# Optimization experiments

Measured on AMD Instinct MI355X. Metric: run time of the kernel, lower is better.

The kernel has to match this reference:

```python
import jax, jax.numpy as jnp
import numpy as np

HIDDEN = 512

def setup_inputs() -> dict:
    key = jax.random.key(0)
    ks = jax.random.split(key, 8)
    S, Bsz, I, H, D = 512, 64, 512, HIDDEN, 2
    return {
        "X": jax.random.normal(ks[0], (S, Bsz, I), jnp.float32),
        "W": jax.random.normal(ks[1], (D, 4 * H, I), jnp.float32) * 0.05,
        "R": jax.random.normal(ks[2], (D, 4 * H, H), jnp.float32) * 0.05,
        "B": jax.random.normal(ks[3], (D, 8 * H), jnp.float32) * 0.05,
        "sequence_lens": jax.random.randint(ks[4], (Bsz,), 0, S, jnp.int32),
        "initial_h": jax.random.normal(ks[5], (D, Bsz, H), jnp.float32) * 0.1,
        "initial_c": jax.random.normal(ks[6], (D, Bsz, H), jnp.float32) * 0.1,
        "P": jax.random.normal(ks[7], (D, 3 * H), jnp.float32) * 0.05,
    }

def _run_dir(Xg, R_d, Rb_d, h0, c0, P_d, seq_lens, ts, H):
    # Gate layout along 4H axis: i, o, f, c (ONNX order used by the source).
    P_i, P_f, P_o = P_d[:H], P_d[H:2 * H], P_d[2 * H:3 * H]

    def step(carry, inp):
        h, c = carry
        xg, t = inp                              # xg: [B,4H] precomputed X@W^T + Wb
        g = xg + h @ R_d.T + Rb_d                # [B,4H]
        i_t = jax.nn.sigmoid(g[:, :H] + P_i * c)
        f_t = jax.nn.sigmoid(g[:, 2 * H:3 * H] + P_f * c)
        c_til = jnp.tanh(g[:, 3 * H:4 * H])
        c_new = f_t * c + i_t * c_til
        o_t = jax.nn.sigmoid(g[:, H:2 * H] + P_o * c_new)
        h_new = o_t * jnp.tanh(c_new)
        mask = (t < seq_lens).astype(h_new.dtype)[:, None]
        h_new = h_new * mask + h0 * (1 - mask)
        c_new = c_new * mask + c0 * (1 - mask)
        return (h_new, c_new), h_new

    (h_f, c_f), hs = jax.lax.scan(step, (h0, c0), (Xg[ts], jnp.asarray(ts)))
    return hs, h_f, c_f

def reference(X, W, R, B, sequence_lens, initial_h, initial_c, P):
    S, Bsz, I = X.shape
    D = W.shape[0]
    H = W.shape[1] // 4
    Wb = B[:, :4 * H]
    Rb = B[:, 4 * H:8 * H]
    # Batch the input projection over all timesteps once: [D,S,B,4H]
    Xg_all = jnp.einsum('sbi,dgi->dsbg', X, W) + Wb[:, None, None, :]
    Ys, Yhs, Ycs = [], [], []
    for d in range(D):
        ts = np.arange(S) if d == 0 else np.arange(S)[::-1].copy()
        hs, h_f, c_f = _run_dir(Xg_all[d], R[d], Rb[d], initial_h[d],
                                initial_c[d], P[d], sequence_lens, ts, H)
        if d == 1:
            hs = hs[::-1]                         # scan emitted reversed time order
        Ys.append(hs)
        Yhs.append(h_f)
        Ycs.append(c_f)
    Y = jnp.stack(Ys, axis=1)                     # [S, D, B, H]
    Y_h = jnp.stack(Yhs, axis=0)                  # [D, B, H]
    Y_c = jnp.stack(Ycs, axis=0)                  # [D, B, H]
    return Y, Y_h, Y_c
```

## Files before the change

kernel.cpp:

```cpp
#include <hip/hip_runtime.h>
#include <stdint.h>
#include <stddef.h>

#define S_LEN 512
#define BATCH 64
#define ISZ   512
#define HID   512
#define NDIR  2

typedef short bf16x8 __attribute__((ext_vector_type(8)));
typedef unsigned short u16x8 __attribute__((ext_vector_type(8)));
typedef float f32x4 __attribute__((ext_vector_type(4)));

#define XB_ELEMS  ((size_t)S_LEN * 4 * 8192)
#define HH_ELEMS  ((size_t)NDIR * 513 * 4 * 8192)
#define CNT_BYTES ((size_t)NDIR * 4 * 513 * 4)
#define XB_BYTES  (XB_ELEMS * 2)
#define HH_BYTES  (HH_ELEMS * 2)

__device__ __forceinline__ unsigned short f2bf(float f) {
    unsigned int u = __float_as_uint(f);
    u += 0x7fffu + ((u >> 16) & 1u);
    return (unsigned short)(u >> 16);
}

__global__ void k_convX(const float* __restrict__ X, unsigned short* __restrict__ Xb) {
    int gu = blockIdx.x * 256 + threadIdx.x;
    int t   = gu >> 12;
    int rem = gu & 4095;
    int b   = rem >> 6;
    int u   = rem & 63;
    const float* src = X + ((size_t)(t * 64 + b)) * 512 + u * 8;
    float4 a = *(const float4*)(src);
    float4 c = *(const float4*)(src + 4);
    u16x8 o;
    o[0]=f2bf(a.x); o[1]=f2bf(a.y); o[2]=f2bf(a.z); o[3]=f2bf(a.w);
    o[4]=f2bf(c.x); o[5]=f2bf(c.y); o[6]=f2bf(c.z); o[7]=f2bf(c.w);
    int i = b >> 4, br = b & 15;
    size_t off = ((size_t)(t * 4 + i)) * 8192 + (size_t)br * 512 + (size_t)((u ^ (b & 7)) << 3);
    *(u16x8*)(Xb + off) = o;
}

__global__ void k_initH(const float* __restrict__ h0, unsigned short* __restrict__ hh) {
    int gu = blockIdx.x * 256 + threadIdx.x;
    int d   = gu >> 12;
    int rem = gu & 4095;
    int b   = rem >> 6;
    int u   = rem & 63;
    const float* src = h0 + ((size_t)(d * 64 + b)) * 512 + u * 8;
    float4 a = *(const float4*)(src);
    float4 c = *(const float4*)(src + 4);
    u16x8 o;
    o[0]=f2bf(a.x); o[1]=f2bf(a.y); o[2]=f2bf(a.z); o[3]=f2bf(a.w);
    o[4]=f2bf(c.x); o[5]=f2bf(c.y); o[6]=f2bf(c.z); o[7]=f2bf(c.w);
    int i = b >> 4, br = b & 15;
    size_t blk = ((size_t)d * 513 + 0) * 4 + i;
    size_t off = blk * 8192 + (size_t)br * 512 + (size_t)((u ^ (b & 7)) << 3);
    *(u16x8*)(hh + off) = o;
}

__launch_bounds__(256, 1)
__global__ void k_lstm(const float* __restrict__ W, const float* __restrict__ R,
                       const float* __restrict__ Bb, const int* __restrict__ slen,
                       const float* __restrict__ h0g, const float* __restrict__ c0g,
                       const float* __restrict__ P,
                       const unsigned short* __restrict__ Xb,
                       unsigned short* __restrict__ hh,
                       int* __restrict__ cnt,
                       float* __restrict__ Y) {
    __shared__ __align__(16) float gbuf[4 * 256];
    __shared__ __align__(4) unsigned short hexch[256];

    const int tid = threadIdx.x;
    const int bx  = blockIdx.x;
    const int d   = bx >> 7;
    const int i   = (bx >> 5) & 3;
    const int j   = bx & 31;
    const int w   = tid >> 6;
    const int l   = tid & 63;
    const int lr  = l & 15;
    const int lq  = l >> 4;

    bf16x8 Wf[16], Rf[16];
    {
        const int row = w * 512 + j * 16 + lr;
        const float* wp = W + ((size_t)(d * 2048 + row)) * 512;
        const float* rp = R + ((size_t)(d * 2048 + row)) * 512;
#pragma unroll
        for (int kc = 0; kc < 16; ++kc) {
            int k0 = kc * 32 + lq * 8;
            float4 a = *(const float4*)(wp + k0);
            float4 b4 = *(const float4*)(wp + k0 + 4);
            bf16x8 f;
            f[0]=(short)f2bf(a.x);  f[1]=(short)f2bf(a.y);  f[2]=(short)f2bf(a.z);  f[3]=(short)f2bf(a.w);
            f[4]=(short)f2bf(b4.x); f[5]=(short)f2bf(b4.y); f[6]=(short)f2bf(b4.z); f[7]=(short)f2bf(b4.w);
            Wf[kc] = f;
            a  = *(const float4*)(rp + k0);
            b4 = *(const float4*)(rp + k0 + 4);
            bf16x8 g;
            g[0]=(short)f2bf(a.x);  g[1]=(short)f2bf(a.y);  g[2]=(short)f2bf(a.z);  g[3]=(short)f2bf(a.w);
            g[4]=(short)f2bf(b4.x); g[5]=(short)f2bf(b4.y); g[6]=(short)f2bf(b4.z); g[7]=(short)f2bf(b4.w);
            Rf[kc] = g;
        }
    }

    const int eb = tid >> 4;
    const int ec = tid & 15;
    const int bg = i * 16 + eb;
    const int kh = j * 16 + ec;
    const float bias_i = Bb[d * 4096 + 0 * 512 + kh] + Bb[d * 4096 + 2048 + 0 * 512 + kh];
    const float bias_o = Bb[d * 4096 + 1 * 512 + kh] + Bb[d * 4096 + 2048 + 1 * 512 + kh];
    const float bias_f = Bb[d * 4096 + 2 * 512 + kh] + Bb[d * 4096 + 2048 + 2 * 512 + kh];
    const float bias_c = Bb[d * 4096 + 3 * 512 + kh] + Bb[d * 4096 + 2048 + 3 * 512 + kh];
    const float Pi = P[d * 1536 + kh];
    const float Pf = P[d * 1536 + 512 + kh];
    const float Po = P[d * 1536 + 1024 + kh];
    const int   sl  = slen[bg];
    const float h0v = h0g[((size_t)d * 64 + bg) * 512 + kh];
    const float c0v = c0g[((size_t)d * 64 + bg) * 512 + kh];
    float c_state = c0v;

    int* mycnt = cnt + (d * 4 + i) * 513;
    const int rbase = lr * 512;
    const int swz   = lr & 7;

    const int peb = tid >> 3;
    const int pm  = tid & 7;
    const size_t puo = (size_t)peb * 256
                     + (size_t)((((2 * j + (pm >> 2)) ^ (peb & 7)) << 2) + (pm & 3));

    for (int ts = 0; ts < 512; ++ts) {
        const int t = (d == 0) ? ts : (511 - ts);

        f32x4 acc = {0.f, 0.f, 0.f, 0.f};
        {
            const unsigned short* xsrc = Xb + ((size_t)(t * 4 + i)) * 8192;
#pragma unroll
            for (int kc = 0; kc < 16; ++kc) {
                int u = (kc * 4 + lq) ^ swz;
                bf16x8 a = *(const bf16x8*)(xsrc + rbase + u * 8);
                acc = __builtin_amdgcn_mfma_f32_16x16x32_bf16(a, Wf[kc], acc, 0, 0, 0);
            }
        }

        if (ts > 0) {
            if (tid == 0) {
                int iters = 0;
                while (__hip_atomic_load(&mycnt[ts], __ATOMIC_RELAXED,
                                         __HIP_MEMORY_SCOPE_AGENT) < 32) {
                    __builtin_amdgcn_s_sleep(1);
                    if (++iters > 4000000) break;
                }
            }
            __syncthreads();
        }

        {
            const unsigned int* hsrc =
                (const unsigned int*)(hh + (((size_t)d * 513 + ts) * 4 + i) * 8192);
            unsigned int hv[64];
#pragma unroll
            for (int kc = 0; kc < 16; ++kc) {
                int u = (kc * 4 + lq) ^ swz;
                const unsigned int* p = hsrc + (lr * 256 + u * 4);
                hv[kc * 4 + 0] = __hip_atomic_load(p + 0, __ATOMIC_RELAXED, __HIP_MEMORY_SCOPE_AGENT);
                hv[kc * 4 + 1] = __hip_atomic_load(p + 1, __ATOMIC_RELAXED, __HIP_MEMORY_SCOPE_AGENT);
                hv[kc * 4 + 2] = __hip_atomic_load(p + 2, __ATOMIC_RELAXED, __HIP_MEMORY_SCOPE_AGENT);
                hv[kc * 4 + 3] = __hip_atomic_load(p + 3, __ATOMIC_RELAXED, __HIP_MEMORY_SCOPE_AGENT);
            }
#pragma unroll
            for (int kc = 0; kc < 16; ++kc) {
                union { unsigned int u[4]; bf16x8 v; } cvt;
                cvt.u[0] = hv[kc * 4 + 0];
                cvt.u[1] = hv[kc * 4 + 1];
                cvt.u[2] = hv[kc * 4 + 2];
                cvt.u[3] = hv[kc * 4 + 3];
                acc = __builtin_amdgcn_mfma_f32_16x16x32_bf16(cvt.v, Rf[kc], acc, 0, 0, 0);
            }
        }

#pragma unroll
        for (int r = 0; r < 4; ++r) {
            int b = lq * 4 + r;
            gbuf[w * 256 + b * 16 + lr] = acc[r];
        }
        __syncthreads();

        float hn, cn;
        {
            float gi = gbuf[0 * 256 + tid] + bias_i;
            float go = gbuf[1 * 256 + tid] + bias_o;
            float gf = gbuf[2 * 256 + tid] + bias_f;
            float gc = gbuf[3 * 256 + tid] + bias_c;
            float c  = c_state;
            float it = 1.f / (1.f + __expf(-(gi + Pi * c)));
            float ft = 1.f / (1.f + __expf(-(gf + Pf * c)));
            float ct = 1.f - 2.f / (__expf(2.f * gc) + 1.f);
            cn = ft * c + it * ct;
            float ot = 1.f / (1.f + __expf(-(go + Po * cn)));
            hn = ot * (1.f - 2.f / (__expf(2.f * cn) + 1.f));
            if (t >= sl) { hn = h0v; cn = c0v; }
            c_state = cn;

            Y[(((size_t)t * 2 + d) * 64 + bg) * 512 + kh] = hn;
            if (ts == 511) {
                Y[(size_t)33554432 + ((size_t)d * 64 + bg) * 512 + kh] = hn;
                Y[(size_t)33619968 + ((size_t)d * 64 + bg) * 512 + kh] = cn;
            }
            hexch[tid] = f2bf(hn);
        }
        __syncthreads();

        if (tid < 128) {
            unsigned int v = ((const unsigned int*)hexch)[tid];
            unsigned int* hdst =
                (unsigned int*)(hh + (((size_t)d * 513 + (ts + 1)) * 4 + i) * 8192);
            __hip_atomic_store(hdst + puo, v, __ATOMIC_RELAXED, __HIP_MEMORY_SCOPE_AGENT);
        }
        asm volatile("s_waitcnt vmcnt(0)" ::: "memory");
        __syncthreads();
        if (tid == 0) {
            __hip_atomic_fetch_add(&mycnt[ts + 1], 1, __ATOMIC_RELAXED,
                                   __HIP_MEMORY_SCOPE_AGENT);
        }
    }
}

extern "C" void kernel_launch(void* const* d_in, const int* in_sizes, int n_in,
                              void* d_out, int out_size, void* d_ws, size_t ws_size,
                              hipStream_t stream) {
    const float* X  = (const float*)d_in[0];
    const float* W  = (const float*)d_in[1];
    const float* R  = (const float*)d_in[2];
    const float* Bb = (const float*)d_in[3];
    const int*   sl = (const int*)d_in[4];
    const float* h0 = (const float*)d_in[5];
    const float* c0 = (const float*)d_in[6];
    const float* P  = (const float*)d_in[7];
    float* Y = (float*)d_out;

    unsigned short* Xb  = (unsigned short*)d_ws;
    unsigned short* hh  = (unsigned short*)((char*)d_ws + XB_BYTES);
    int*            cnt = (int*)((char*)d_ws + XB_BYTES + HH_BYTES);

    hipMemsetAsync(cnt, 0, CNT_BYTES, stream);

    k_convX<<<8192, 256, 0, stream>>>(X, Xb);
    k_initH<<<32, 256, 0, stream>>>(h0, hh);
    k_lstm<<<256, 256, 0, stream>>>(W, R, Bb, sl, h0, c0, P, Xb, hh, cnt, Y);
}
```

Baseline: 4.082 ms.

## Remap LSTM blocks by XCD so each group syncs through its local L2

At kernel start each block reads its hardware XCD id, all blocks meet at a global barrier, and roles are reassigned so that each 32-block group exchanging hidden state sits on the same XCD. When that grouping succeeds, the per-step hidden-state exchange and counter polling use plain loads, stores and workgroup-scope atomics that stay in the XCD's L2, instead of agent-scope atomics that go through device-coherent memory. The per-step counter becomes one monotonically increasing counter per group, and the LDS staging of h is replaced by a lane shuffle that packs bf16 pairs. This adds a startup rendezvous that depends on all 256 blocks being resident at once, and the fast path's correctness relies on the assumption that same-XCD blocks share a coherent L2.

```diff
diff --git a/kernel.cpp b/kernel.cpp
--- a/kernel.cpp
+++ b/kernel.cpp
@@ -14,7 +14,7 @@
 
 #define XB_ELEMS  ((size_t)S_LEN * 4 * 8192)
 #define HH_ELEMS  ((size_t)NDIR * 513 * 4 * 8192)
-#define CNT_BYTES ((size_t)NDIR * 4 * 513 * 4)
+#define CNT_BYTES ((size_t)16416)
 #define XB_BYTES  (XB_ELEMS * 2)
 #define HH_BYTES  (HH_ELEMS * 2)
 
@@ -22,6 +22,14 @@
     unsigned int u = __float_as_uint(f);
     u += 0x7fffu + ((u >> 16) & 1u);
     return (unsigned short)(u >> 16);
+}
+
+__device__ __forceinline__ int l2_load_i32(const int* p) {
+    int v;
+    asm volatile("global_load_dword %0, %1, off sc0\n\t"
+                 "s_waitcnt vmcnt(0)"
+                 : "=v"(v) : "v"(p) : "memory");
+    return v;
 }
 
 __global__ void k_convX(const float* __restrict__ X, unsigned short* __restrict__ Xb) {
@@ -69,17 +77,63 @@
                        int* __restrict__ cnt,
                        float* __restrict__ Y) {
     __shared__ __align__(16) float gbuf[4 * 256];
-    __shared__ __align__(4) unsigned short hexch[256];
+    __shared__ int s_xcd[256];
+    __shared__ unsigned char s_inv[256];
+    __shared__ int s_role, s_fast;
 
     const int tid = threadIdx.x;
     const int bx  = blockIdx.x;
-    const int d   = bx >> 7;
-    const int i   = (bx >> 5) & 3;
-    const int j   = bx & 31;
-    const int w   = tid >> 6;
-    const int l   = tid & 63;
-    const int lr  = l & 15;
-    const int lq  = l >> 4;
+
+    int* const arrive = cnt;
+    int* const xcdtab = cnt + 288;
+
+    if (tid == 0) {
+        int x;
+        asm volatile("s_getreg_b32 %0, hwreg(HW_REG_XCC_ID)" : "=s"(x));
+        x &= 0xf;
+        __hip_atomic_store(&xcdtab[bx], x + 1, __ATOMIC_RELAXED, __HIP_MEMORY_SCOPE_AGENT);
+        asm volatile("s_waitcnt vmcnt(0)" ::: "memory");
+        __hip_atomic_fetch_add(arrive, 1, __ATOMIC_RELAXED, __HIP_MEMORY_SCOPE_AGENT);
+        int iters = 0;
+        while (__hip_atomic_load(arrive, __ATOMIC_RELAXED, __HIP_MEMORY_SCOPE_AGENT) < 256) {
+            __builtin_amdgcn_s_sleep(1);
+            if (++iters > 2000000) break;
+        }
+    }
+    __syncthreads();
+    s_xcd[tid] = __hip_atomic_load(&xcdtab[tid], __ATOMIC_RELAXED, __HIP_MEMORY_SCOPE_AGENT) - 1;
+    __syncthreads();
+    {
+        const int myx = s_xcd[tid];
+        int r = 0;
+        for (int b = 0; b < 256; ++b) {
+            const int xb = s_xcd[b];
+            r += (int)((xb < myx) | ((xb == myx) & (b < tid)));
+        }
+        s_inv[r] = (unsigned char)(myx & 0xff);
+        if (tid == bx) s_role = r;
+    }
+    __syncthreads();
+    if (tid == 0) {
+        const int g0 = s_role & ~31;
+        int uni = 1;
+        for (int q = 1; q < 32; ++q) uni &= (int)(s_inv[g0 + q] == s_inv[g0]);
+        int distinct = 1;
+        for (int q = 1; q < 256; ++q) distinct += (int)(s_inv[q] != s_inv[q - 1]);
+        s_fast = uni & (int)(distinct >= 2);
+    }
+    __syncthreads();
+    const int  role = s_role;
+    const bool fast = (s_fast != 0);
+    const int  d = role >> 7;
+    const int  i = (role >> 5) & 3;
+    const int  j = role & 31;
+    int* const gcnt = cnt + 32 + ((role >> 5) << 5);
+
+    const int w  = tid >> 6;
+    const int l  = tid & 63;
+    const int lr = l & 15;
+    const int lq = l >> 4;
 
     bf16x8 Wf[16], Rf[16];
     {
@@ -120,14 +174,13 @@
     const float c0v = c0g[((size_t)d * 64 + bg) * 512 + kh];
     float c_state = c0v;
 
-    int* mycnt = cnt + (d * 4 + i) * 513;
     const int rbase = lr * 512;
     const int swz   = lr & 7;
 
-    const int peb = tid >> 3;
-    const int pm  = tid & 7;
+    const int peb = tid >> 4;
+    const int cp  = (tid & 15) >> 1;
     const size_t puo = (size_t)peb * 256
-                     + (size_t)((((2 * j + (pm >> 2)) ^ (peb & 7)) << 2) + (pm & 3));
+                     + (size_t)((((2 * j + (cp >> 2)) ^ (peb & 7)) << 2) + (cp & 3));
 
     for (int ts = 0; ts < 512; ++ts) {
         const int t = (d == 0) ? ts : (511 - ts);
@@ -145,37 +198,57 @@
 
         if (ts > 0) {
             if (tid == 0) {
+                const int target = 32 * ts;
                 int iters = 0;
-                while (__hip_atomic_load(&mycnt[ts], __ATOMIC_RELAXED,
-                                         __HIP_MEMORY_SCOPE_AGENT) < 32) {
-                    __builtin_amdgcn_s_sleep(1);
-                    if (++iters > 4000000) break;
+                if (fast) {
+                    while (l2_load_i32(gcnt) < target) {
+                        __builtin_amdgcn_s_sleep(1);
+                        if (++iters > 4000000) break;
+                    }
+                } else {
+                    while (__hip_atomic_load(gcnt, __ATOMIC_RELAXED,
+                                             __HIP_MEMORY_SCOPE_AGENT) < target) {
+                        __builtin_amdgcn_s_sleep(1);
+                        if (++iters > 4000000) break;
+                    }
                 }
             }
             __syncthreads();
         }
 
         {
-            const unsigned int* hsrc =
-                (const unsigned int*)(hh + (((size_t)d * 513 + ts) * 4 + i) * 8192);
-            unsigned int hv[64];
-#pragma unroll
-            for (int kc = 0; kc < 16; ++kc) {
-                int u = (kc * 4 + lq) ^ swz;
-                const unsigned int* p = hsrc + (lr * 256 + u * 4);
-                hv[kc * 4 + 0] = __hip_atomic_load(p + 0, __ATOMIC_RELAXED, __HIP_MEMORY_SCOPE_AGENT);
-                hv[kc * 4 + 1] = __hip_atomic_load(p + 1, __ATOMIC_RELAXED, __HIP_MEMORY_SCOPE_AGENT);
-                hv[kc * 4 + 2] = __hip_atomic_load(p + 2, __ATOMIC_RELAXED, __HIP_MEMORY_SCOPE_AGENT);
-                hv[kc * 4 + 3] = __hip_atomic_load(p + 3, __ATOMIC_RELAXED, __HIP_MEMORY_SCOPE_AGENT);
-            }
-#pragma unroll
-            for (int kc = 0; kc < 16; ++kc) {
-                union { unsigned int u[4]; bf16x8 v; } cvt;
-                cvt.u[0] = hv[kc * 4 + 0];
-                cvt.u[1] = hv[kc * 4 + 1];
-                cvt.u[2] = hv[kc * 4 + 2];
-                cvt.u[3] = hv[kc * 4 + 3];
-                acc = __builtin_amdgcn_mfma_f32_16x16x32_bf16(cvt.v, Rf[kc], acc, 0, 0, 0);
+            const unsigned short* hsrc16 = hh + (((size_t)d * 513 + ts) * 4 + i) * 8192;
+            if (fast) {
+                bf16x8 hf[16];
+#pragma unroll
+                for (int kc = 0; kc < 16; ++kc) {
+                    const int u = (kc * 4 + lq) ^ swz;
+                    hf[kc] = *(const bf16x8*)(hsrc16 + rbase + u * 8);
+                }
+#pragma unroll
+                for (int kc = 0; kc < 16; ++kc)
+                    acc = __builtin_amdgcn_mfma_f32_16x16x32_bf16(hf[kc], Rf[kc], acc, 0, 0, 0);
+            } else {
+                const unsigned int* hsrc = (const unsigned int*)hsrc16;
+                unsigned int hv[64];
+#pragma unroll
+                for (int kc = 0; kc < 16; ++kc) {
+                    int u = (kc * 4 + lq) ^ swz;
+                    const unsigned int* p = hsrc + (lr * 256 + u * 4);
+                    hv[kc * 4 + 0] = __hip_atomic_load(p + 0, __ATOMIC_RELAXED, __HIP_MEMORY_SCOPE_AGENT);
+                    hv[kc * 4 + 1] = __hip_atomic_load(p + 1, __ATOMIC_RELAXED, __HIP_MEMORY_SCOPE_AGENT);
+                    hv[kc * 4 + 2] = __hip_atomic_load(p + 2, __ATOMIC_RELAXED, __HIP_MEMORY_SCOPE_AGENT);
+                    hv[kc * 4 + 3] = __hip_atomic_load(p + 3, __ATOMIC_RELAXED, __HIP_MEMORY_SCOPE_AGENT);
+                }
+#pragma unroll
+                for (int kc = 0; kc < 16; ++kc) {
+                    union { unsigned int u[4]; bf16x8 v; } cvt;
+                    cvt.u[0] = hv[kc * 4 + 0];
+                    cvt.u[1] = hv[kc * 4 + 1];
+                    cvt.u[2] = hv[kc * 4 + 2];
+                    cvt.u[3] = hv[kc * 4 + 3];
+                    acc = __builtin_amdgcn_mfma_f32_16x16x32_bf16(cvt.v, Rf[kc], acc, 0, 0, 0);
+                }
             }
         }
 
@@ -207,21 +280,27 @@
                 Y[(size_t)33554432 + ((size_t)d * 64 + bg) * 512 + kh] = hn;
                 Y[(size_t)33619968 + ((size_t)d * 64 + bg) * 512 + kh] = cn;
             }
-            hexch[tid] = f2bf(hn);
-        }
-        __syncthreads();
-
-        if (tid < 128) {
-            unsigned int v = ((const unsigned int*)hexch)[tid];
-            unsigned int* hdst =
-                (unsigned int*)(hh + (((size_t)d * 513 + (ts + 1)) * 4 + i) * 8192);
-            __hip_atomic_store(hdst + puo, v, __ATOMIC_RELAXED, __HIP_MEMORY_SCOPE_AGENT);
+        }
+
+        {
+            const unsigned int hb = (unsigned int)f2bf(hn);
+            const unsigned int other = (unsigned int)__shfl_xor((int)hb, 1);
+            if ((tid & 1) == 0) {
+                const unsigned int v = hb | (other << 16);
+                unsigned int* hdst =
+                    (unsigned int*)(hh + (((size_t)d * 513 + (ts + 1)) * 4 + i) * 8192);
+                if (fast) hdst[puo] = v;
+                else __hip_atomic_store(hdst + puo, v, __ATOMIC_RELAXED,
+                                        __HIP_MEMORY_SCOPE_AGENT);
+            }
         }
         asm volatile("s_waitcnt vmcnt(0)" ::: "memory");
         __syncthreads();
         if (tid == 0) {
-            __hip_atomic_fetch_add(&mycnt[ts + 1], 1, __ATOMIC_RELAXED,
-                                   __HIP_MEMORY_SCOPE_AGENT);
+            if (fast) __hip_atomic_fetch_add(gcnt, 1, __ATOMIC_RELAXED,
+                                             __HIP_MEMORY_SCOPE_WORKGROUP);
+            else      __hip_atomic_fetch_add(gcnt, 1, __ATOMIC_RELAXED,
+                                             __HIP_MEMORY_SCOPE_AGENT);
         }
     }
 }
```

After: 3.837 ms. 1.06x faster.
